# Optimization experiments

Hardware: AMD Instinct MI355X
Metric: run time of the kernel (lower is better)

The kernel has to match this reference:

```python
import jax, jax.numpy as jnp
import numpy as np

B, L, CIN, COUT, HEADS = 8, 2048, 256, 256, 4
HD = COUT // HEADS
NEG_SLOPE = 0.2


def setup_inputs() -> dict:
    key = jax.random.key(0)
    k1, k2, k3, k4, k5 = jax.random.split(key, 5)
    x = jax.random.normal(k1, (B, L, CIN), dtype=jnp.float32)
    adj_mask = jax.random.randint(k2, (B, L, L), 0, 2) > 0  # bool [B,L,L]
    W = jax.random.normal(k3, (COUT, CIN), dtype=jnp.float32) * (1.0 / np.sqrt(CIN))
    att_src = jax.random.normal(k4, (1, HEADS, 1, HD), dtype=jnp.float32) * 0.1
    att_dst = jax.random.normal(k5, (1, HEADS, 1, HD), dtype=jnp.float32) * 0.1
    return {"x": x, "adj_mask": adj_mask, "W": W, "att_src": att_src, "att_dst": att_dst}


def reference(x, adj_mask, W, att_src, att_dst):
    Bb, Ll, _ = x.shape
    # linear projection (no bias), split heads: [B, H, L, D]
    h = jnp.einsum('blc,oc->blo', x, W).reshape(Bb, Ll, HEADS, HD).transpose(0, 2, 1, 3)
    # additive GAT scores
    a_src = jnp.sum(h * att_src, axis=-1, keepdims=True)          # [B,H,L,1]
    a_dst = jnp.sum(h * att_dst, axis=-1, keepdims=True)          # [B,H,L,1]
    e = a_src + jnp.swapaxes(a_dst, 2, 3)                          # [B,H,L,L]
    e = jnp.where(e >= 0, e, NEG_SLOPE * e)                        # leaky relu
    fill = jnp.finfo(e.dtype).min
    e = jnp.where(adj_mask[:, None, :, :], e, fill)                # mask non-edges
    alpha = jax.nn.softmax(e, axis=-1)                             # [B,H,L,L]
    # dropout is identity in eval/reference mode
    out = jnp.einsum('bhij,bhjd->bhid', alpha, h)                  # [B,H,L,D]
    return out.transpose(0, 2, 1, 3).reshape(Bb, Ll, COUT)
```

## Files before the change

### kernel.cpp

```cpp
#include <hip/hip_runtime.h>

#define B_ 8
#define L_ 2048
#define CIN_ 256
#define COUT_ 256
#define HEADS_ 4
#define HD_ 64
#define NEG_SLOPE_ 0.2f
#define LOG2E_ 1.4426950408889634f

#define TI 32
#define TJ 64
#define NJT (L_ / TJ)

typedef __attribute__((ext_vector_type(4))) float f32x4;
typedef __attribute__((ext_vector_type(8))) __bf16 bf16x8;
typedef __attribute__((ext_vector_type(4))) __bf16 bf16x4;


__global__ __launch_bounds__(256, 4)
void pack_kernel(const int* __restrict__ adj, unsigned long long* __restrict__ abitsT) {
  const size_t wid = ((size_t)blockIdx.x * 256 + threadIdx.x) >> 6;
  const int lane = threadIdx.x & 63;
  const int* p = adj + wid * 256 + lane;
  unsigned long long b0 = __ballot(p[0]   != 0);
  unsigned long long b1 = __ballot(p[64]  != 0);
  unsigned long long b2 = __ballot(p[128] != 0);
  unsigned long long b3 = __ballot(p[192] != 0);
  if (lane == 0) {
    const size_t row = wid >> 3;
    const int jw0 = (int)(wid & 7) * 4;
    const size_t bb = row >> 11, l = row & 2047;
    unsigned long long* dst = abitsT + (bb << 16) + l;
    dst[(size_t)(jw0 + 0) << 11] = b0;
    dst[(size_t)(jw0 + 1) << 11] = b1;
    dst[(size_t)(jw0 + 2) << 11] = b2;
    dst[(size_t)(jw0 + 3) << 11] = b3;
  }
}

__global__ __launch_bounds__(256, 2)
void proj_kernel(const float* __restrict__ x, const float* __restrict__ W,
                 const float* __restrict__ att_src, const float* __restrict__ att_dst,
                 __bf16* __restrict__ hF, float2* __restrict__ aE,
                 float2* __restrict__ aF) {
  __shared__ __align__(16) __bf16 Wl[COUT_][80];
  __shared__ __align__(16) __bf16 Al[2][2][512];

  const int tid = threadIdx.x;
  const int r0 = blockIdx.x * TI;
  const int b  = r0 >> 11;
  const int l0 = r0 & (L_ - 1);

  const int w = tid >> 6, lane = tid & 63, col = lane & 15, q = lane >> 4;
  const int si = tid >> 3, soct = tid & 7;
  const int wn = tid >> 2, wkq = tid & 3;

  f32x4 acc[2][4];
#pragma unroll
  for (int mt = 0; mt < 2; ++mt)
#pragma unroll
    for (int nt = 0; nt < 4; ++nt) acc[mt][nt] = (f32x4)0.f;

  for (int kc = 0; kc < CIN_ / 64; ++kc) {
    __syncthreads();
#pragma unroll
    for (int rg = 0; rg < 4; ++rg) {
      const int row = rg * 64 + wn;
      const float4* ws = (const float4*)(W + (size_t)row * CIN_ + kc * 64 + wkq * 16);
#pragma unroll
      for (int u = 0; u < 4; ++u) {
        float4 f = ws[u];
        bf16x4 v;
        v[0] = (__bf16)f.x; v[1] = (__bf16)f.y; v[2] = (__bf16)f.z; v[3] = (__bf16)f.w;
        *(bf16x4*)&Wl[row][wkq * 16 + u * 4] = v;
      }
    }
    {
      const float4* xs = (const float4*)(x + (size_t)(r0 + si) * CIN_ + kc * 64 + soct * 8);
      float4 f0 = xs[0], f1 = xs[1];
      bf16x8 v;
      v[0] = (__bf16)f0.x; v[1] = (__bf16)f0.y; v[2] = (__bf16)f0.z; v[3] = (__bf16)f0.w;
      v[4] = (__bf16)f1.x; v[5] = (__bf16)f1.y; v[6] = (__bf16)f1.z; v[7] = (__bf16)f1.w;
      *(bf16x8*)&Al[si >> 4][soct >> 2][(((soct & 3) << 4) + (si & 15)) << 3] = v;
    }
    __syncthreads();

    bf16x8 af[2][2], bfr[2][4];
#pragma unroll
    for (int mt = 0; mt < 2; ++mt)
#pragma unroll
      for (int kt = 0; kt < 2; ++kt)
        af[mt][kt] = *(const bf16x8*)&Al[mt][kt][lane << 3];
#pragma unroll
    for (int kt = 0; kt < 2; ++kt)
#pragma unroll
      for (int nt = 0; nt < 4; ++nt)
        bfr[kt][nt] = *(const bf16x8*)&Wl[w * 64 + nt * 16 + col][kt * 32 + q * 8];
#pragma unroll
    for (int kt = 0; kt < 2; ++kt)
#pragma unroll
      for (int mt = 0; mt < 2; ++mt)
#pragma unroll
        for (int nt = 0; nt < 4; ++nt)
          acc[mt][nt] = __builtin_amdgcn_mfma_f32_16x16x32_bf16(
              af[mt][kt], bfr[kt][nt], acc[mt][nt], 0, 0, 0);
  }

  float asv[4], adv[4];
#pragma unroll
  for (int nt = 0; nt < 4; ++nt) {
    asv[nt] = att_src[w * 64 + nt * 16 + col];
    adv[nt] = att_dst[w * 64 + nt * 16 + col];
  }
#pragma unroll
  for (int mt = 0; mt < 2; ++mt)
#pragma unroll
    for (int reg = 0; reg < 4; ++reg) {
      float s = 0.f, d = 0.f;
#pragma unroll
      for (int nt = 0; nt < 4; ++nt) {
        s = fmaf(acc[mt][nt][reg], asv[nt], s);
        d = fmaf(acc[mt][nt][reg], adv[nt], d);
      }
      s += __shfl_xor(s, 1, 64); d += __shfl_xor(d, 1, 64);
      s += __shfl_xor(s, 2, 64); d += __shfl_xor(d, 2, 64);
      s += __shfl_xor(s, 4, 64); d += __shfl_xor(d, 4, 64);
      s += __shfl_xor(s, 8, 64); d += __shfl_xor(d, 8, 64);
      if (col == 0) {
        int il = mt * 16 + q * 4 + reg;
        const size_t idx = ((size_t)(b * HEADS_ + w) << 11) + l0 + il;
        float2 ev, fv;
        ev.x = __builtin_exp2f(s * LOG2E_);
        ev.y = __builtin_exp2f(s * (LOG2E_ * NEG_SLOPE_));
        fv.x = __builtin_exp2f(d * LOG2E_);
        fv.y = __builtin_exp2f(d * (LOG2E_ * NEG_SLOPE_));
        aE[idx] = ev;
        aF[idx] = fv;
      }
    }

  {
    const int jt_p = l0 >> 6;
    const int kt_p = (l0 >> 5) & 1;
    const int qhi = q >> 1, qlo = q & 1;
#pragma unroll
    for (int mt = 0; mt < 2; ++mt) {
      const int qp = mt * 2 + qhi;
#pragma unroll
      for (int nt = 0; nt < 4; ++nt) {
        bf16x4 v;
        v[0] = (__bf16)acc[mt][nt][0];
        v[1] = (__bf16)acc[mt][nt][1];
        v[2] = (__bf16)acc[mt][nt][2];
        v[3] = (__bf16)acc[mt][nt][3];
        const size_t off =
            ((((size_t)(b * HEADS_ + w) * 32 + jt_p) * 2 + kt_p) * 4 + nt) * 512 +
            (qp * 16 + col) * 8 + qlo * 4;
        *(bf16x4*)(hF + off) = v;
      }
    }
  }
}

__global__ __launch_bounds__(512)
void attn_kernel(const __bf16* __restrict__ hF, const float2* __restrict__ aE,
                 const float2* __restrict__ aF,
                 const unsigned long long* __restrict__ abitsT,
                 float* __restrict__ out) {
  __shared__ __align__(16) float comb[HEADS_][64][40];

  const int tid = threadIdx.x;
  const int b  = blockIdx.x & 7;
  const int i0 = (blockIdx.x >> 3) * 32;

  const int w = tid >> 6, lane = tid & 63, col = lane & 15, q = lane >> 4;
  const int hh = w & 3;
  const int jh = w >> 2;
  const int jt0 = jh * (NJT / 2), jt1 = jt0 + NJT / 2;

  const size_t hl = (size_t)(b * HEADS_ + hh);
  const float2 EE[2] = {aE[(hl << 11) + i0 + col],
                        aE[(hl << 11) + i0 + 16 + col]};
  const float* afb = (const float*)(aF + (hl << 11)) + q * 16;
  const __bf16* hb = hF + hl * 131072 + lane * 8;
  const unsigned long long* mb = abitsT + ((size_t)b << 16) + i0 + col;

  bf16x8 bones;
#pragma unroll
  for (int e = 0; e < 8; ++e) bones[e] = (__bf16)1.0f;

  f32x4 acc[2][4], accl[2];
#pragma unroll
  for (int mt = 0; mt < 2; ++mt) {
    accl[mt] = (f32x4)0.f;
#pragma unroll
    for (int nt = 0; nt < 4; ++nt) acc[mt][nt] = (f32x4)0.f;
  }

  unsigned long long cm0 = mb[(size_t)jt0 << 11];
  unsigned long long cm1 = mb[((size_t)jt0 << 11) + 16];

  for (int jt = jt0; jt < jt1; ++jt) {
    const int jn = (jt < jt1 - 1) ? jt + 1 : jt;
    const unsigned long long nm0 = mb[(size_t)jn << 11];
    const unsigned long long nm1 = mb[((size_t)jn << 11) + 16];

#pragma unroll
    for (int kt = 0; kt < 2; ++kt) {
      bf16x8 cb0 = *(const bf16x8*)(hb + jt * 4096 + (kt * 4 + 0) * 512);
      bf16x8 cb1 = *(const bf16x8*)(hb + jt * 4096 + (kt * 4 + 1) * 512);
      bf16x8 cb2 = *(const bf16x8*)(hb + jt * 4096 + (kt * 4 + 2) * 512);
      bf16x8 cb3 = *(const bf16x8*)(hb + jt * 4096 + (kt * 4 + 3) * 512);
      float cf[16];
#pragma unroll
      for (int u = 0; u < 4; ++u)
        *(float4*)&cf[u * 4] =
            *(const float4*)(afb + jt * 128 + kt * 64 + u * 4);

      bf16x8 av[2];
#pragma unroll
      for (int mt = 0; mt < 2; ++mt) {
        const unsigned long long bw = mt ? cm1 : cm0;
        const unsigned int tsh = ((unsigned int)(bw >> (kt * 32))) >> (q * 8);
        const float Ex = EE[mt].x, Ey = EE[mt].y;
#pragma unroll
        for (int e = 0; e < 8; ++e) {
          const float m1 = Ex * cf[2 * e];
          const float m2 = Ey * cf[2 * e + 1];
          const float pm = fmaxf(m1, m2);
          const float p = (tsh & (1u << e)) ? pm : 0.f;
          av[mt][e] = (__bf16)p;
        }
      }
#pragma unroll
      for (int mt = 0; mt < 2; ++mt) {
        acc[mt][0] = __builtin_amdgcn_mfma_f32_16x16x32_bf16(av[mt], cb0, acc[mt][0], 0, 0, 0);
        acc[mt][1] = __builtin_amdgcn_mfma_f32_16x16x32_bf16(av[mt], cb1, acc[mt][1], 0, 0, 0);
        acc[mt][2] = __builtin_amdgcn_mfma_f32_16x16x32_bf16(av[mt], cb2, acc[mt][2], 0, 0, 0);
        acc[mt][3] = __builtin_amdgcn_mfma_f32_16x16x32_bf16(av[mt], cb3, acc[mt][3], 0, 0, 0);
        accl[mt] = __builtin_amdgcn_mfma_f32_16x16x32_bf16(av[mt], bones, accl[mt], 0, 0, 0);
      }
    }

    cm0 = nm0; cm1 = nm1;
  }

  if (jh == 1) {
#pragma unroll
    for (int mt = 0; mt < 2; ++mt)
#pragma unroll
      for (int nt = 0; nt < 4; ++nt)
        *(f32x4*)&comb[hh][lane][mt * 16 + nt * 4] = acc[mt][nt];
    *(f32x4*)&comb[hh][lane][32] = accl[0];
    *(f32x4*)&comb[hh][lane][36] = accl[1];
  }
  __syncthreads();
  if (jh == 0) {
#pragma unroll
    for (int mt = 0; mt < 2; ++mt) {
      const f32x4 lo = accl[mt] + *(const f32x4*)&comb[hh][lane][32 + mt * 4];
#pragma unroll
      for (int reg = 0; reg < 4; ++reg) {
        const int m = q * 4 + reg;
        const float linv = 1.0f / lo[reg];
        const size_t orow =
            ((size_t)(b * L_ + i0 + mt * 16 + m)) * COUT_ + hh * 64;
#pragma unroll
        for (int nt = 0; nt < 4; ++nt) {
          const float v =
              acc[mt][nt][reg] + comb[hh][lane][mt * 16 + nt * 4 + reg];
          out[orow + nt * 16 + col] = v * linv;
        }
      }
    }
  }
}

extern "C" void kernel_launch(void* const* d_in, const int* in_sizes, int n_in,
                              void* d_out, int out_size, void* d_ws, size_t ws_size,
                              hipStream_t stream) {
  const float* x       = (const float*)d_in[0];
  const int*   adj     = (const int*)d_in[1];
  const float* W       = (const float*)d_in[2];
  const float* att_src = (const float*)d_in[3];
  const float* att_dst = (const float*)d_in[4];
  float* out = (float*)d_out;

  char* ws = (char*)d_ws;
  __bf16* hF = (__bf16*)ws;
  float2* aE = (float2*)(ws + (8u << 20));
  float2* aF = (float2*)(ws + (9u << 20));
  unsigned long long* abitsT =
      (unsigned long long*)(ws + (10u << 20));

  pack_kernel<<<(B_ * L_ * (L_ / 256)) / 4, 256, 0, stream>>>(adj, abitsT);
  proj_kernel<<<(B_ * L_) / TI, 256, 0, stream>>>(x, W, att_src, att_dst, hF, aE, aF);
  attn_kernel<<<B_ * (L_ / 32), 512, 0, stream>>>(hF, aE, aF, abitsT, out);
}
```

Before: 261.2 us.

## Replace row-sum MFMA with scalar sums, widen projection block to 8 waves

The attention kernel drops the extra MFMA against a ones vector that computed softmax denominators. It accumulates row sums with scalar adds plus cross-lane shuffles instead, and stops prefetching the next mask word, which frees registers and MFMA issue slots. The projection kernel moves to 512 threads, with each wave covering one head and one 16-row half, so per-thread accumulators halve and the W staging is spread across more threads. LDS padding shrinks in both kernels. The risks are lost latency hiding for the mask loads and a different summation order for the denominator, which is now taken from the fp32 p values rather than the bf16-rounded ones.

```diff
diff --git a/kernel.cpp b/kernel.cpp
--- a/kernel.cpp
+++ b/kernel.cpp
@@ -39,12 +39,12 @@
   }
 }
 
-__global__ __launch_bounds__(256, 2)
+__global__ __launch_bounds__(512, 2)
 void proj_kernel(const float* __restrict__ x, const float* __restrict__ W,
                  const float* __restrict__ att_src, const float* __restrict__ att_dst,
                  __bf16* __restrict__ hF, float2* __restrict__ aE,
                  float2* __restrict__ aF) {
-  __shared__ __align__(16) __bf16 Wl[COUT_][80];
+  __shared__ __align__(16) __bf16 Wl[COUT_][72];
   __shared__ __align__(16) __bf16 Al[2][2][512];
 
   const int tid = threadIdx.x;
@@ -52,31 +52,32 @@
   const int b  = r0 >> 11;
   const int l0 = r0 & (L_ - 1);
 
-  const int w = tid >> 6, lane = tid & 63, col = lane & 15, q = lane >> 4;
+  const int w8 = tid >> 6, lane = tid & 63, col = lane & 15, q = lane >> 4;
+  const int h  = w8 & 3;
+  const int mh = w8 >> 2;
+  const int wrow = tid >> 3;
+  const int wc8  = (tid & 7) * 8;
   const int si = tid >> 3, soct = tid & 7;
-  const int wn = tid >> 2, wkq = tid & 3;
-
-  f32x4 acc[2][4];
-#pragma unroll
-  for (int mt = 0; mt < 2; ++mt)
-#pragma unroll
-    for (int nt = 0; nt < 4; ++nt) acc[mt][nt] = (f32x4)0.f;
+
+  f32x4 acc[4];
+#pragma unroll
+  for (int nt = 0; nt < 4; ++nt) acc[nt] = (f32x4)0.f;
 
   for (int kc = 0; kc < CIN_ / 64; ++kc) {
     __syncthreads();
 #pragma unroll
     for (int rg = 0; rg < 4; ++rg) {
-      const int row = rg * 64 + wn;
-      const float4* ws = (const float4*)(W + (size_t)row * CIN_ + kc * 64 + wkq * 16);
-#pragma unroll
-      for (int u = 0; u < 4; ++u) {
+      const int row = rg * 64 + wrow;
+      const float4* ws = (const float4*)(W + (size_t)row * CIN_ + kc * 64 + wc8);
+#pragma unroll
+      for (int u = 0; u < 2; ++u) {
         float4 f = ws[u];
         bf16x4 v;
         v[0] = (__bf16)f.x; v[1] = (__bf16)f.y; v[2] = (__bf16)f.z; v[3] = (__bf16)f.w;
-        *(bf16x4*)&Wl[row][wkq * 16 + u * 4] = v;
-      }
-    }
-    {
+        *(bf16x4*)&Wl[row][wc8 + u * 4] = v;
+      }
+    }
+    if (tid < 256) {
       const float4* xs = (const float4*)(x + (size_t)(r0 + si) * CIN_ + kc * 64 + soct * 8);
       float4 f0 = xs[0], f1 = xs[1];
       bf16x8 v;
@@ -86,89 +87,80 @@
     }
     __syncthreads();
 
-    bf16x8 af[2][2], bfr[2][4];
-#pragma unroll
-    for (int mt = 0; mt < 2; ++mt)
-#pragma unroll
-      for (int kt = 0; kt < 2; ++kt)
-        af[mt][kt] = *(const bf16x8*)&Al[mt][kt][lane << 3];
+    bf16x8 af[2], bfr[2][4];
 #pragma unroll
     for (int kt = 0; kt < 2; ++kt)
+      af[kt] = *(const bf16x8*)&Al[mh][kt][lane << 3];
+#pragma unroll
+    for (int kt = 0; kt < 2; ++kt)
 #pragma unroll
       for (int nt = 0; nt < 4; ++nt)
-        bfr[kt][nt] = *(const bf16x8*)&Wl[w * 64 + nt * 16 + col][kt * 32 + q * 8];
+        bfr[kt][nt] = *(const bf16x8*)&Wl[h * 64 + nt * 16 + col][kt * 32 + q * 8];
 #pragma unroll
     for (int kt = 0; kt < 2; ++kt)
 #pragma unroll
-      for (int mt = 0; mt < 2; ++mt)
-#pragma unroll
-        for (int nt = 0; nt < 4; ++nt)
-          acc[mt][nt] = __builtin_amdgcn_mfma_f32_16x16x32_bf16(
-              af[mt][kt], bfr[kt][nt], acc[mt][nt], 0, 0, 0);
+      for (int nt = 0; nt < 4; ++nt)
+        acc[nt] = __builtin_amdgcn_mfma_f32_16x16x32_bf16(
+            af[kt], bfr[kt][nt], acc[nt], 0, 0, 0);
   }
 
   float asv[4], adv[4];
 #pragma unroll
   for (int nt = 0; nt < 4; ++nt) {
-    asv[nt] = att_src[w * 64 + nt * 16 + col];
-    adv[nt] = att_dst[w * 64 + nt * 16 + col];
-  }
-#pragma unroll
-  for (int mt = 0; mt < 2; ++mt)
-#pragma unroll
-    for (int reg = 0; reg < 4; ++reg) {
-      float s = 0.f, d = 0.f;
-#pragma unroll
-      for (int nt = 0; nt < 4; ++nt) {
-        s = fmaf(acc[mt][nt][reg], asv[nt], s);
-        d = fmaf(acc[mt][nt][reg], adv[nt], d);
-      }
-      s += __shfl_xor(s, 1, 64); d += __shfl_xor(d, 1, 64);
-      s += __shfl_xor(s, 2, 64); d += __shfl_xor(d, 2, 64);
-      s += __shfl_xor(s, 4, 64); d += __shfl_xor(d, 4, 64);
-      s += __shfl_xor(s, 8, 64); d += __shfl_xor(d, 8, 64);
-      if (col == 0) {
-        int il = mt * 16 + q * 4 + reg;
-        const size_t idx = ((size_t)(b * HEADS_ + w) << 11) + l0 + il;
-        float2 ev, fv;
-        ev.x = __builtin_exp2f(s * LOG2E_);
-        ev.y = __builtin_exp2f(s * (LOG2E_ * NEG_SLOPE_));
-        fv.x = __builtin_exp2f(d * LOG2E_);
-        fv.y = __builtin_exp2f(d * (LOG2E_ * NEG_SLOPE_));
-        aE[idx] = ev;
-        aF[idx] = fv;
-      }
-    }
+    asv[nt] = att_src[h * 64 + nt * 16 + col];
+    adv[nt] = att_dst[h * 64 + nt * 16 + col];
+  }
+#pragma unroll
+  for (int reg = 0; reg < 4; ++reg) {
+    float s = 0.f, d = 0.f;
+#pragma unroll
+    for (int nt = 0; nt < 4; ++nt) {
+      s = fmaf(acc[nt][reg], asv[nt], s);
+      d = fmaf(acc[nt][reg], adv[nt], d);
+    }
+    s += __shfl_xor(s, 1, 64); d += __shfl_xor(d, 1, 64);
+    s += __shfl_xor(s, 2, 64); d += __shfl_xor(d, 2, 64);
+    s += __shfl_xor(s, 4, 64); d += __shfl_xor(d, 4, 64);
+    s += __shfl_xor(s, 8, 64); d += __shfl_xor(d, 8, 64);
+    if (col == 0) {
+      const int il = mh * 16 + q * 4 + reg;
+      const size_t idx = ((size_t)(b * HEADS_ + h) << 11) + l0 + il;
+      float2 ev, fv;
+      ev.x = __builtin_exp2f(s * LOG2E_);
+      ev.y = __builtin_exp2f(s * (LOG2E_ * NEG_SLOPE_));
+      fv.x = __builtin_exp2f(d * LOG2E_);
+      fv.y = __builtin_exp2f(d * (LOG2E_ * NEG_SLOPE_));
+      aE[idx] = ev;
+      aF[idx] = fv;
+    }
+  }
 
   {
     const int jt_p = l0 >> 6;
     const int kt_p = (l0 >> 5) & 1;
     const int qhi = q >> 1, qlo = q & 1;
-#pragma unroll
-    for (int mt = 0; mt < 2; ++mt) {
-      const int qp = mt * 2 + qhi;
-#pragma unroll
-      for (int nt = 0; nt < 4; ++nt) {
-        bf16x4 v;
-        v[0] = (__bf16)acc[mt][nt][0];
-        v[1] = (__bf16)acc[mt][nt][1];
-        v[2] = (__bf16)acc[mt][nt][2];
-        v[3] = (__bf16)acc[mt][nt][3];
-        const size_t off =
-            ((((size_t)(b * HEADS_ + w) * 32 + jt_p) * 2 + kt_p) * 4 + nt) * 512 +
-            (qp * 16 + col) * 8 + qlo * 4;
-        *(bf16x4*)(hF + off) = v;
-      }
-    }
-  }
-}
-
-__global__ __launch_bounds__(512)
+    const int qp = mh * 2 + qhi;
+#pragma unroll
+    for (int nt = 0; nt < 4; ++nt) {
+      bf16x4 v;
+      v[0] = (__bf16)acc[nt][0];
+      v[1] = (__bf16)acc[nt][1];
+      v[2] = (__bf16)acc[nt][2];
+      v[3] = (__bf16)acc[nt][3];
+      const size_t off =
+          ((((size_t)(b * HEADS_ + h) * 32 + jt_p) * 2 + kt_p) * 4 + nt) * 512 +
+          (qp * 16 + col) * 8 + qlo * 4;
+      *(bf16x4*)(hF + off) = v;
+    }
+  }
+}
+
+__global__ __launch_bounds__(512, 2)
 void attn_kernel(const __bf16* __restrict__ hF, const float2* __restrict__ aE,
                  const float2* __restrict__ aF,
                  const unsigned long long* __restrict__ abitsT,
                  float* __restrict__ out) {
-  __shared__ __align__(16) float comb[HEADS_][64][40];
+  __shared__ __align__(16) float comb[HEADS_][64][36];
 
   const int tid = threadIdx.x;
   const int b  = blockIdx.x & 7;
@@ -186,25 +178,16 @@
   const __bf16* hb = hF + hl * 131072 + lane * 8;
   const unsigned long long* mb = abitsT + ((size_t)b << 16) + i0 + col;
 
-  bf16x8 bones;
-#pragma unroll
-  for (int e = 0; e < 8; ++e) bones[e] = (__bf16)1.0f;
-
-  f32x4 acc[2][4], accl[2];
-#pragma unroll
-  for (int mt = 0; mt < 2; ++mt) {
-    accl[mt] = (f32x4)0.f;
+  f32x4 acc[2][4];
+  float lsum[2] = {0.f, 0.f};
+#pragma unroll
+  for (int mt = 0; mt < 2; ++mt)
 #pragma unroll
     for (int nt = 0; nt < 4; ++nt) acc[mt][nt] = (f32x4)0.f;
-  }
-
-  unsigned long long cm0 = mb[(size_t)jt0 << 11];
-  unsigned long long cm1 = mb[((size_t)jt0 << 11) + 16];
 
   for (int jt = jt0; jt < jt1; ++jt) {
-    const int jn = (jt < jt1 - 1) ? jt + 1 : jt;
-    const unsigned long long nm0 = mb[(size_t)jn << 11];
-    const unsigned long long nm1 = mb[((size_t)jn << 11) + 16];
+    const unsigned long long cm0 = mb[(size_t)jt << 11];
+    const unsigned long long cm1 = mb[((size_t)jt << 11) + 16];
 
 #pragma unroll
     for (int kt = 0; kt < 2; ++kt) {
@@ -224,14 +207,17 @@
         const unsigned long long bw = mt ? cm1 : cm0;
         const unsigned int tsh = ((unsigned int)(bw >> (kt * 32))) >> (q * 8);
         const float Ex = EE[mt].x, Ey = EE[mt].y;
+        float part = 0.f;
 #pragma unroll
         for (int e = 0; e < 8; ++e) {
           const float m1 = Ex * cf[2 * e];
           const float m2 = Ey * cf[2 * e + 1];
           const float pm = fmaxf(m1, m2);
           const float p = (tsh & (1u << e)) ? pm : 0.f;
+          part += p;
           av[mt][e] = (__bf16)p;
         }
+        lsum[mt] += part;
       }
 #pragma unroll
       for (int mt = 0; mt < 2; ++mt) {
@@ -239,11 +225,14 @@
         acc[mt][1] = __builtin_amdgcn_mfma_f32_16x16x32_bf16(av[mt], cb1, acc[mt][1], 0, 0, 0);
         acc[mt][2] = __builtin_amdgcn_mfma_f32_16x16x32_bf16(av[mt], cb2, acc[mt][2], 0, 0, 0);
         acc[mt][3] = __builtin_amdgcn_mfma_f32_16x16x32_bf16(av[mt], cb3, acc[mt][3], 0, 0, 0);
-        accl[mt] = __builtin_amdgcn_mfma_f32_16x16x32_bf16(av[mt], bones, accl[mt], 0, 0, 0);
-      }
-    }
-
-    cm0 = nm0; cm1 = nm1;
+      }
+    }
+  }
+
+#pragma unroll
+  for (int mt = 0; mt < 2; ++mt) {
+    lsum[mt] += __shfl_xor(lsum[mt], 16, 64);
+    lsum[mt] += __shfl_xor(lsum[mt], 32, 64);
   }
 
   if (jh == 1) {
@@ -252,18 +241,19 @@
 #pragma unroll
       for (int nt = 0; nt < 4; ++nt)
         *(f32x4*)&comb[hh][lane][mt * 16 + nt * 4] = acc[mt][nt];
-    *(f32x4*)&comb[hh][lane][32] = accl[0];
-    *(f32x4*)&comb[hh][lane][36] = accl[1];
+    comb[hh][lane][32] = lsum[0];
+    comb[hh][lane][33] = lsum[1];
   }
   __syncthreads();
   if (jh == 0) {
 #pragma unroll
     for (int mt = 0; mt < 2; ++mt) {
-      const f32x4 lo = accl[mt] + *(const f32x4*)&comb[hh][lane][32 + mt * 4];
+      const float ltot = lsum[mt] + comb[hh][lane][32 + mt];
 #pragma unroll
       for (int reg = 0; reg < 4; ++reg) {
         const int m = q * 4 + reg;
-        const float linv = 1.0f / lo[reg];
+        const float lm = __shfl(ltot, m, 64);
+        const float linv = 1.0f / lm;
         const size_t orow =
             ((size_t)(b * L_ + i0 + mt * 16 + m)) * COUT_ + hh * 64;
 #pragma unroll
@@ -295,6 +285,6 @@
       (unsigned long long*)(ws + (10u << 20));
 
   pack_kernel<<<(B_ * L_ * (L_ / 256)) / 4, 256, 0, stream>>>(adj, abitsT);
-  proj_kernel<<<(B_ * L_) / TI, 256, 0, stream>>>(x, W, att_src, att_dst, hF, aE, aF);
+  proj_kernel<<<(B_ * L_) / TI, 512, 0, stream>>>(x, W, att_src, att_dst, hF, aE, aF);
   attn_kernel<<<B_ * (L_ / 32), 512, 0, stream>>>(hF, aE, aF, abitsT, out);
 }
```

After: 263.3 us. About the same (+0.8%).
